# Kernel optimization log

Measured on AMD Instinct MI355X. Metric: run time of the kernel, lower is better.

The kernel has to match this reference:

```python
import jax, jax.numpy as jnp
import numpy as np

N_NODES = 50000
N_EDGES = 800000
DIM = 128


def setup_inputs() -> dict:
    key = jax.random.key(0)
    k1, k2, k3, k4, k5 = jax.random.split(key, 5)
    X = jax.random.normal(k1, (N_NODES, DIM), dtype=jnp.float32)
    src = jax.random.randint(k2, (N_EDGES,), 0, N_NODES, dtype=jnp.int64)
    dst = jax.random.randint(k3, (N_EDGES,), 0, N_NODES, dtype=jnp.int64)
    W_self = jax.random.normal(k4, (DIM, DIM), dtype=jnp.float32) * (1.0 / np.sqrt(DIM))
    W_neigh = jax.random.normal(k5, (DIM, DIM), dtype=jnp.float32) * (1.0 / np.sqrt(DIM))
    bias = jnp.zeros((DIM,), dtype=jnp.float32)
    return {"X": X, "src": src, "dst": dst, "W_self": W_self, "W_neigh": W_neigh, "bias": bias}


def reference(X, src, dst, W_self, W_neigh, bias):
    # h[u] = ReLU(W_self x_u + sum_{v in N(u)} W_neigh x_v + b)
    # Transform once per node, then gather per edge and segment-sum into dst.
    h_self = X @ W_self.T                       # [N, out]
    xw = X @ W_neigh.T                          # [N, out]
    h_neigh = jax.ops.segment_sum(xw[src], dst, num_segments=N_NODES)  # [N, out]
    return jax.nn.relu(h_self + h_neigh + bias)
```

## Files before the change

kernel.cpp:

```cpp
#include <hip/hip_runtime.h>
#include <hip/hip_bf16.h>

#define NN 50000
#define NE 800000
#define DIM 128
#define NBLK 49

#define NBUCK 196
#define CAP   6144
#define EPB   3200
#define PBLK  250

typedef __attribute__((ext_vector_type(8))) short bf16x8;
typedef __attribute__((ext_vector_type(4))) float f32x4;

__device__ __forceinline__ short f2bf(float f) {
    union { float f; unsigned u; } x; x.f = f;
    unsigned r = x.u + 0x7fffu + ((x.u >> 16) & 1u);
    return (short)(r >> 16);
}

__device__ __forceinline__ bf16x8 pack8(float4 a, float4 b) {
    bf16x8 v;
    v[0] = f2bf(a.x); v[1] = f2bf(a.y); v[2] = f2bf(a.z); v[3] = f2bf(a.w);
    v[4] = f2bf(b.x); v[5] = f2bf(b.y); v[6] = f2bf(b.z); v[7] = f2bf(b.w);
    return v;
}

__device__ __forceinline__ float bf2f(short s) {
    union { unsigned u; float f; } x; x.u = ((unsigned)(unsigned short)s) << 16;
    return x.f;
}

__device__ __forceinline__ void acc8(f32x4& aA, f32x4& aB, bf16x8 x) {
    aA[0] += bf2f(x[0]); aA[1] += bf2f(x[1]); aA[2] += bf2f(x[2]); aA[3] += bf2f(x[3]);
    aB[0] += bf2f(x[4]); aB[1] += bf2f(x[5]); aB[2] += bf2f(x[6]); aB[3] += bf2f(x[7]);
}

__global__ __launch_bounds__(256) void zero_k(int* __restrict__ p) {
    p[threadIdx.x] = 0;
}


__global__ __launch_bounds__(256) void part1(const float* __restrict__ X,
                                             const int* __restrict__ src,
                                             const int* __restrict__ dst,
                                             short* __restrict__ Xb,
                                             int* __restrict__ bucketFill,
                                             unsigned* __restrict__ edges) {
    __shared__ unsigned stage[EPB];
    __shared__ unsigned sorted_[EPB];
    __shared__ int lcnt[256];
    __shared__ int lst[256];
    __shared__ int goff[256];
    __shared__ int c2[256];

    int b = blockIdx.x;
    int t = threadIdx.x;

    if (b < 3125) {
        int i = b * 256 + t;
        const float4* p = (const float4*)(X + (size_t)i * 8);
        *(bf16x8*)(Xb + (size_t)i * 8) = pack8(p[0], p[1]);
        return;
    }

    int pb = b - 3125;
    int e0 = pb * EPB;
    lcnt[t] = 0; c2[t] = 0;
    __syncthreads();

    for (int i = t * 4; i < EPB; i += 1024) {
        int4 s4 = *(const int4*)(src + e0 + i);
        int4 d4 = *(const int4*)(dst + e0 + i);
        int ss[4] = {s4.x, s4.y, s4.z, s4.w};
        int dd[4] = {d4.x, d4.y, d4.z, d4.w};
        #pragma unroll
        for (int j = 0; j < 4; ++j) {
            unsigned bk = (unsigned)dd[j] >> 8;
            unsigned dl = (unsigned)dd[j] & 255u;
            stage[i + j] = (bk << 24) | (dl << 16) | (unsigned)ss[j];
            atomicAdd(&lcnt[bk], 1);
        }
    }
    __syncthreads();

    int v = lcnt[t];
    for (int off = 1; off < 256; off <<= 1) {
        __syncthreads();
        int tmp = (t >= off) ? lcnt[t - off] : 0;
        __syncthreads();
        lcnt[t] += tmp;
    }
    __syncthreads();
    int excl = lcnt[t] - v;
    lst[t] = excl;
    if (t < NBUCK) {
        int gb = atomicAdd(&bucketFill[t], v);
        goff[t] = t * CAP + gb - excl;
    }
    __syncthreads();

    for (int i = t * 4; i < EPB; i += 1024) {
        uint4 p4 = *(const uint4*)&stage[i];
        unsigned pp[4] = {p4.x, p4.y, p4.z, p4.w};
        #pragma unroll
        for (int j = 0; j < 4; ++j) {
            int bj = pp[j] >> 24;
            int r = atomicAdd(&c2[bj], 1);
            sorted_[lst[bj] + r] = pp[j];
        }
    }
    __syncthreads();

    for (int i = t * 4; i < EPB; i += 1024) {
        uint4 p4 = *(const uint4*)&sorted_[i];
        unsigned pp[4] = {p4.x, p4.y, p4.z, p4.w};
        #pragma unroll
        for (int j = 0; j < 4; ++j) {
            int bj = pp[j] >> 24;
            edges[(size_t)goff[bj] + i + j] = pp[j];
        }
    }
}

__global__ __launch_bounds__(256) void pull2(const short* __restrict__ Xb,
                                             const int* __restrict__ bucketFill,
                                             const unsigned* __restrict__ edges,
                                             short* __restrict__ aggb) {
    __shared__ int cnt[32];
    __shared__ int c2s[32];
    __shared__ int start[33];
    __shared__ unsigned short lcsr[1024];

    int t = threadIdx.x;
    int b  = blockIdx.x >> 3;
    int sl = blockIdx.x & 7;
    int dlo = sl * 32;
    int m = bucketFill[b];
    const unsigned* ed = edges + (size_t)b * CAP;

    if (t < 32) { cnt[t] = 0; c2s[t] = 0; }
    __syncthreads();

    for (int i = t * 4; i < m; i += 1024) {
        if (i + 4 <= m) {
            uint4 e4 = *(const uint4*)(ed + i);
            unsigned pp[4] = {e4.x, e4.y, e4.z, e4.w};
            #pragma unroll
            for (int j = 0; j < 4; ++j) {
                int o = ((pp[j] >> 16) & 255u) - dlo;
                if ((unsigned)o < 32u) atomicAdd(&cnt[o], 1);
            }
        } else {
            for (int k = i; k < m; ++k) {
                int o = ((ed[k] >> 16) & 255u) - dlo;
                if ((unsigned)o < 32u) atomicAdd(&cnt[o], 1);
            }
        }
    }
    __syncthreads();

    int v = (t < 32) ? cnt[t] : 0;
    for (int off = 1; off < 32; off <<= 1) {
        __syncthreads();
        int tmp = (t >= off && t < 32) ? cnt[t - off] : 0;
        __syncthreads();
        if (t < 32) cnt[t] += tmp;
    }
    __syncthreads();
    if (t < 32) start[t] = cnt[t] - v;
    if (t == 31) start[32] = cnt[31];
    __syncthreads();

    for (int i = t * 4; i < m; i += 1024) {
        if (i + 4 <= m) {
            uint4 e4 = *(const uint4*)(ed + i);
            unsigned pp[4] = {e4.x, e4.y, e4.z, e4.w};
            #pragma unroll
            for (int j = 0; j < 4; ++j) {
                int o = ((pp[j] >> 16) & 255u) - dlo;
                if ((unsigned)o < 32u) {
                    int r = atomicAdd(&c2s[o], 1);
                    lcsr[start[o] + r] = (unsigned short)(pp[j] & 0xffffu);
                }
            }
        } else {
            for (int k = i; k < m; ++k) {
                unsigned p = ed[k];
                int o = ((p >> 16) & 255u) - dlo;
                if ((unsigned)o < 32u) {
                    int r = atomicAdd(&c2s[o], 1);
                    lcsr[start[o] + r] = (unsigned short)(p & 0xffffu);
                }
            }
        }
    }
    __syncthreads();

    int lane = t & 63, wv = t >> 6;
    int g = lane >> 4, fl = lane & 15;
    const short* xbase = Xb + fl * 8;
    for (int n = wv; n < 32; n += 4) {
        int u = (b << 8) + dlo + n;
        if (u >= NN) continue;
        int beg = start[n], end = start[n + 1];
        f32x4 aA = {0.f, 0.f, 0.f, 0.f}, aB = {0.f, 0.f, 0.f, 0.f};
        int e = beg;
        for (; e + 16 <= end; e += 16) {
            int v0 = lcsr[e + g];
            int v1 = lcsr[e + 4 + g];
            int v2 = lcsr[e + 8 + g];
            int v3 = lcsr[e + 12 + g];
            bf16x8 x0 = *(const bf16x8*)(xbase + (size_t)v0 * DIM);
            bf16x8 x1 = *(const bf16x8*)(xbase + (size_t)v1 * DIM);
            bf16x8 x2 = *(const bf16x8*)(xbase + (size_t)v2 * DIM);
            bf16x8 x3 = *(const bf16x8*)(xbase + (size_t)v3 * DIM);
            acc8(aA, aB, x0); acc8(aA, aB, x1);
            acc8(aA, aB, x2); acc8(aA, aB, x3);
        }
        for (; e + 8 <= end; e += 8) {
            int v0 = lcsr[e + g];
            int v1 = lcsr[e + 4 + g];
            bf16x8 x0 = *(const bf16x8*)(xbase + (size_t)v0 * DIM);
            bf16x8 x1 = *(const bf16x8*)(xbase + (size_t)v1 * DIM);
            acc8(aA, aB, x0); acc8(aA, aB, x1);
        }
        for (; e < end; e += 4) {
            int idx = e + g;
            int vv = lcsr[idx < end ? idx : beg];
            bf16x8 x = *(const bf16x8*)(xbase + (size_t)vv * DIM);
            if (idx < end) acc8(aA, aB, x);
        }
        #pragma unroll
        for (int i = 0; i < 4; ++i) {
            aA[i] += __shfl_xor(aA[i], 16); aA[i] += __shfl_xor(aA[i], 32);
            aB[i] += __shfl_xor(aB[i], 16); aB[i] += __shfl_xor(aB[i], 32);
        }
        if (g == 0) {
            bf16x8 r;
            r[0] = f2bf(aA[0]); r[1] = f2bf(aA[1]); r[2] = f2bf(aA[2]); r[3] = f2bf(aA[3]);
            r[4] = f2bf(aB[0]); r[5] = f2bf(aB[1]); r[6] = f2bf(aB[2]); r[7] = f2bf(aB[3]);
            *(bf16x8*)(aggb + (size_t)u * DIM + fl * 8) = r;
        }
    }
}

__global__ __launch_bounds__(512) void gemm_bb(const short* __restrict__ Xb,
                                               const short* __restrict__ aggb,
                                               const float* __restrict__ Ws,
                                               const float* __restrict__ Wn,
                                               const float* __restrict__ bias,
                                               float* __restrict__ out) {
    __shared__ __align__(16) short wlds[2][128][128];
    for (int i = threadIdx.x; i < 128 * 16; i += 512) {
        int row = i >> 4;
        int c8 = (i & 15) << 3;
        int sc = c8 ^ ((row & 15) << 3);
        const float4* ps = (const float4*)(Ws + row * DIM + c8);
        *(bf16x8*)&wlds[0][row][sc] = pack8(ps[0], ps[1]);
        const float4* pn = (const float4*)(Wn + row * DIM + c8);
        *(bf16x8*)&wlds[1][row][sc] = pack8(pn[0], pn[1]);
    }
    __syncthreads();

    int lane = threadIdx.x & 63;
    int wv = threadIdx.x >> 6;
    int n0 = blockIdx.x * 128 + wv * 16;
    int arow = n0 + (lane & 15);
    int rowc = arow < NN ? arow : (NN - 1);
    const short* xr = Xb   + (size_t)rowc * DIM + (lane >> 4) * 8;
    const short* ar = aggb + (size_t)rowc * DIM + (lane >> 4) * 8;

    f32x4 acc[8] = {};
    #pragma unroll
    for (int ks = 0; ks < 4; ++ks) {
        int k0 = ks * 32;
        bf16x8 afx = *(const bf16x8*)(xr + k0);
        bf16x8 afg = *(const bf16x8*)(ar + k0);
        int bcol = k0 + (lane >> 4) * 8;
        #pragma unroll
        for (int ot = 0; ot < 8; ++ot) {
            int brow = ot * 16 + (lane & 15);
            int sc = bcol ^ ((brow & 15) << 3);
            bf16x8 bs = *(const bf16x8*)&wlds[0][brow][sc];
            bf16x8 bn = *(const bf16x8*)&wlds[1][brow][sc];
            acc[ot] = __builtin_amdgcn_mfma_f32_16x16x32_bf16(afx, bs, acc[ot], 0, 0, 0);
            acc[ot] = __builtin_amdgcn_mfma_f32_16x16x32_bf16(afg, bn, acc[ot], 0, 0, 0);
        }
    }

    int col0 = lane & 15;
    int rbase = n0 + (lane >> 4) * 4;
    #pragma unroll
    for (int ot = 0; ot < 8; ++ot) {
        int col = ot * 16 + col0;
        float bv = bias[col];
        #pragma unroll
        for (int i = 0; i < 4; ++i) {
            int r = rbase + i;
            if (r < NN) out[(size_t)r * DIM + col] = fmaxf(acc[ot][i] + bv, 0.f);
        }
    }
}


__global__ __launch_bounds__(256) void hist_k(const int* __restrict__ dst,
                                              int* __restrict__ cnt) {
    int e = blockIdx.x * 256 + threadIdx.x;
    if (e < NE) atomicAdd(&cnt[dst[e]], 1);
}

__global__ __launch_bounds__(1024) void scanA(const int* __restrict__ cnt,
                                              int* __restrict__ rowstart,
                                              int* __restrict__ bsum) {
    __shared__ int s[1024];
    int i = blockIdx.x * 1024 + threadIdx.x;
    int v = (i < NN) ? cnt[i] : 0;
    s[threadIdx.x] = v;
    for (int off = 1; off < 1024; off <<= 1) {
        __syncthreads();
        int t = (threadIdx.x >= off) ? s[threadIdx.x - off] : 0;
        __syncthreads();
        s[threadIdx.x] += t;
    }
    __syncthreads();
    if (i < NN) rowstart[i] = s[threadIdx.x] - v;
    if (threadIdx.x == 1023) bsum[blockIdx.x] = s[1023];
}

__global__ __launch_bounds__(64) void scanB(int* __restrict__ bsum) {
    int l = threadIdx.x;
    int orig = (l < NBLK) ? bsum[l] : 0;
    int v = orig;
    for (int off = 1; off < 64; off <<= 1) {
        int t = __shfl_up(v, off);
        if (l >= off) v += t;
    }
    if (l < NBLK) bsum[l] = v - orig;
}

__global__ __launch_bounds__(1024) void scanC(int* __restrict__ rowstart,
                                              const int* __restrict__ bsum) {
    int i = blockIdx.x * 1024 + threadIdx.x;
    if (i < NN) rowstart[i] += bsum[blockIdx.x];
    if (i == 0) rowstart[NN] = NE;
}

__global__ __launch_bounds__(256) void fill_atomic(const int* __restrict__ src,
                                                   const int* __restrict__ dst,
                                                   int* __restrict__ rowstart,
                                                   int* __restrict__ csr) {
    int e = blockIdx.x * 256 + threadIdx.x;
    if (e < NE) {
        int p = atomicAdd(&rowstart[dst[e]], 1);
        csr[p] = src[e];
    }
}

__global__ __launch_bounds__(256) void cvt_k(const float* __restrict__ X,
                                             short* __restrict__ Xb) {
    int i = blockIdx.x * 256 + threadIdx.x;
    if (i < NN * DIM / 8) {
        const float4* p = (const float4*)(X + (size_t)i * 8);
        *(bf16x8*)(Xb + (size_t)i * 8) = pack8(p[0], p[1]);
    }
}

__global__ __launch_bounds__(256) void pull_bf16(const short* __restrict__ Xb,
                                                 const int* __restrict__ rowend,
                                                 const int* __restrict__ csr,
                                                 float* __restrict__ agg) {
    int lane = threadIdx.x & 63;
    int u = (blockIdx.x * 256 + threadIdx.x) >> 6;
    if (u >= NN) return;
    int beg = (u == 0) ? 0 : rowend[u - 1];
    int end = rowend[u];
    float2 a0 = {0.f, 0.f}, a1 = {0.f, 0.f};
    int e = beg;
    for (; e + 1 < end; e += 2) {
        int v0 = csr[e], v1 = csr[e + 1];
        ushort2 x0 = *(const ushort2*)(Xb + (size_t)v0 * DIM + lane * 2);
        ushort2 x1 = *(const ushort2*)(Xb + (size_t)v1 * DIM + lane * 2);
        a0.x += bf2f(x0.x); a0.y += bf2f(x0.y);
        a1.x += bf2f(x1.x); a1.y += bf2f(x1.y);
    }
    if (e < end) {
        int v0 = csr[e];
        ushort2 x0 = *(const ushort2*)(Xb + (size_t)v0 * DIM + lane * 2);
        a0.x += bf2f(x0.x); a0.y += bf2f(x0.y);
    }
    float2 r = {a0.x + a1.x, a0.y + a1.y};
    *(float2*)(agg + (size_t)u * DIM + lane * 2) = r;
}

__global__ __launch_bounds__(256) void scatter_k(const float* __restrict__ X,
                                                 const int* __restrict__ src,
                                                 const int* __restrict__ dst,
                                                 float* __restrict__ agg) {
    int lane = threadIdx.x & 63;
    int gw = (blockIdx.x * 256 + threadIdx.x) >> 6;
    int nw = (gridDim.x * 256) >> 6;
    for (int e = gw; e < NE; e += nw) {
        int s = src[e];
        int d = dst[e];
        float2 v = *(const float2*)(X + (size_t)s * DIM + lane * 2);
        float* a = agg + (size_t)d * DIM + lane * 2;
        unsafeAtomicAdd(a, v.x);
        unsafeAtomicAdd(a + 1, v.y);
    }
}

__global__ __launch_bounds__(256) void fused_gemm(
        const float* __restrict__ X,
        const float* __restrict__ agg,
        const float* __restrict__ Ws,
        const float* __restrict__ Wn,
        const float* __restrict__ bias,
        float* __restrict__ out) {
    __shared__ __align__(16) short wlds[2][128][128];
    for (int i = threadIdx.x; i < 128 * 16; i += 256) {
        int row = i >> 4;
        int c8 = (i & 15) << 3;
        int sc = c8 ^ ((row & 15) << 3);
        const float4* ps = (const float4*)(Ws + row * DIM + c8);
        *(bf16x8*)&wlds[0][row][sc] = pack8(ps[0], ps[1]);
        const float4* pn = (const float4*)(Wn + row * DIM + c8);
        *(bf16x8*)&wlds[1][row][sc] = pack8(pn[0], pn[1]);
    }
    __syncthreads();

    int lane = threadIdx.x & 63;
    int wv = threadIdx.x >> 6;
    int n0 = blockIdx.x * 64 + wv * 16;
    int arow = n0 + (lane & 15);
    int rowc = arow < NN ? arow : (NN - 1);
    const float* xr = X + (size_t)rowc * DIM + (lane >> 4) * 8;
    const float* ar = agg + (size_t)rowc * DIM + (lane >> 4) * 8;

    f32x4 acc[8] = {};
    #pragma unroll
    for (int ks = 0; ks < 4; ++ks) {
        int k0 = ks * 32;
        float4 xa = *(const float4*)(xr + k0);
        float4 xb = *(const float4*)(xr + k0 + 4);
        bf16x8 afx = pack8(xa, xb);
        float4 ga = *(const float4*)(ar + k0);
        float4 gb = *(const float4*)(ar + k0 + 4);
        bf16x8 afg = pack8(ga, gb);
        int bcol = k0 + (lane >> 4) * 8;
        #pragma unroll
        for (int ot = 0; ot < 8; ++ot) {
            int brow = ot * 16 + (lane & 15);
            int sc = bcol ^ ((brow & 15) << 3);
            bf16x8 bs = *(const bf16x8*)&wlds[0][brow][sc];
            bf16x8 bn = *(const bf16x8*)&wlds[1][brow][sc];
            acc[ot] = __builtin_amdgcn_mfma_f32_16x16x32_bf16(afx, bs, acc[ot], 0, 0, 0);
            acc[ot] = __builtin_amdgcn_mfma_f32_16x16x32_bf16(afg, bn, acc[ot], 0, 0, 0);
        }
    }

    int col0 = lane & 15;
    int rbase = n0 + (lane >> 4) * 4;
    #pragma unroll
    for (int ot = 0; ot < 8; ++ot) {
        int col = ot * 16 + col0;
        float bv = bias[col];
        #pragma unroll
        for (int i = 0; i < 4; ++i) {
            int r = rbase + i;
            if (r < NN) out[(size_t)r * DIM + col] = fmaxf(acc[ot][i] + bv, 0.f);
        }
    }
}


extern "C" void kernel_launch(void* const* d_in, const int* in_sizes, int n_in,
                              void* d_out, int out_size, void* d_ws, size_t ws_size,
                              hipStream_t stream) {
    const float* X    = (const float*)d_in[0];
    const int*   src  = (const int*)  d_in[1];
    const int*   dst  = (const int*)  d_in[2];
    const float* Ws   = (const float*)d_in[3];
    const float* Wn   = (const float*)d_in[4];
    const float* bias = (const float*)d_in[5];
    float* out = (float*)d_out;

    const size_t REQ0 = ((size_t)256 + (size_t)NBUCK * CAP
                      + (size_t)NN * DIM / 2 * 2) * 4;
    const size_t REQ2 = (size_t)(50048 + 50056 + 64 + 800000) * 4
                      + (size_t)NN * DIM * 2;

    if (ws_size >= REQ0) {
        int*      bf    = (int*)d_ws;
        unsigned* edges = (unsigned*)(bf + 256);
        short*    Xb    = (short*)(edges + (size_t)NBUCK * CAP);
        short*    aggb  = Xb + (size_t)NN * DIM;

        zero_k<<<1, 256, 0, stream>>>(bf);
        part1<<<3125 + PBLK, 256, 0, stream>>>(X, src, dst, Xb, bf, edges);
        pull2<<<NBUCK * 8, 256, 0, stream>>>(Xb, bf, edges, aggb);
        gemm_bb<<<(NN + 127) / 128, 512, 0, stream>>>(Xb, aggb, Ws, Wn, bias, out);
    } else if (ws_size >= REQ2) {
        int* cnt      = (int*)d_ws;
        int* rowstart = cnt + 50048;
        int* bsum     = rowstart + 50056;
        int* csr      = bsum + 64;
        short* Xb     = (short*)(csr + 800000);

        hipMemsetAsync(cnt, 0, 50048 * sizeof(int), stream);
        hist_k<<<3125, 256, 0, stream>>>(dst, cnt);
        scanA<<<NBLK, 1024, 0, stream>>>(cnt, rowstart, bsum);
        scanB<<<1, 64, 0, stream>>>(bsum);
        scanC<<<NBLK, 1024, 0, stream>>>(rowstart, bsum);
        fill_atomic<<<3125, 256, 0, stream>>>(src, dst, rowstart, csr);
        cvt_k<<<3125, 256, 0, stream>>>(X, Xb);
        pull_bf16<<<12500, 256, 0, stream>>>(Xb, rowstart, csr, out);
        fused_gemm<<<(NN + 63) / 64, 256, 0, stream>>>(X, out, Ws, Wn, bias, out);
    } else {
        hipMemsetAsync(out, 0, (size_t)NN * DIM * sizeof(float), stream);
        scatter_k<<<2048, 256, 0, stream>>>(X, src, dst, out);
        fused_gemm<<<(NN + 63) / 64, 256, 0, stream>>>(X, out, Ws, Wn, bias, out);
    }
}
```

Before: 76.09 us.

## Fuse neighbor aggregation with dual GEMM, keep aggregates in LDS

Merges the pull aggregation kernel and the GEMM kernel into one pullgemm kernel. Each block now handles 64 destination nodes, keeps the bf16 aggregates in swizzled shared memory, and runs the self and neighbor MFMA passes one after the other. The weights are converted to bf16 once, by two extra blocks in part1, and reloaded into a single shared buffer between the two passes. This removes the global write and re-read of the aggregate tensor and one launch. In exchange it uses more shared memory per block and adds a capped local CSR (LCAP) that could silently drop edges when a 64-node slice has more than 1536 incoming edges.

```diff
diff --git a/kernel.cpp b/kernel.cpp
--- a/kernel.cpp
+++ b/kernel.cpp
@@ -10,6 +10,7 @@
 #define CAP   6144
 #define EPB   3200
 #define PBLK  250
+#define LCAP  1536
 
 typedef __attribute__((ext_vector_type(8))) short bf16x8;
 typedef __attribute__((ext_vector_type(4))) float f32x4;
@@ -45,7 +46,10 @@
 __global__ __launch_bounds__(256) void part1(const float* __restrict__ X,
                                              const int* __restrict__ src,
                                              const int* __restrict__ dst,
+                                             const float* __restrict__ Ws,
+                                             const float* __restrict__ Wn,
                                              short* __restrict__ Xb,
+                                             short* __restrict__ Wb,
                                              int* __restrict__ bucketFill,
                                              unsigned* __restrict__ edges) {
     __shared__ unsigned stage[EPB];
@@ -64,6 +68,18 @@
         *(bf16x8*)(Xb + (size_t)i * 8) = pack8(p[0], p[1]);
         return;
     }
+    if (b >= 3375) {
+        int w = b - 3375;
+        const float* Wsrc = (w == 0) ? Ws : Wn;
+        for (int i = t; i < 2048; i += 256) {
+            int row = i >> 4;
+            int c8 = (i & 15) << 3;
+            int sc = c8 ^ ((row & 15) << 3);
+            const float4* p = (const float4*)(Wsrc + row * DIM + c8);
+            *(bf16x8*)(Wb + (size_t)w * 16384 + row * 128 + sc) = pack8(p[0], p[1]);
+        }
+        return;
+    }
 
     int pb = b - 3125;
     int e0 = pb * EPB;
@@ -124,23 +140,28 @@
     }
 }
 
-__global__ __launch_bounds__(256) void pull2(const short* __restrict__ Xb,
-                                             const int* __restrict__ bucketFill,
-                                             const unsigned* __restrict__ edges,
-                                             short* __restrict__ aggb) {
-    __shared__ int cnt[32];
-    __shared__ int c2s[32];
-    __shared__ int start[33];
-    __shared__ unsigned short lcsr[1024];
+__global__ __launch_bounds__(256, 3) void pullgemm(
+        const short* __restrict__ Xb,
+        const short* __restrict__ Wb,
+        const int* __restrict__ bucketFill,
+        const unsigned* __restrict__ edges,
+        const float* __restrict__ bias,
+        float* __restrict__ out) {
+    __shared__ __align__(16) short wlds[128][128];
+    __shared__ __align__(16) short agg[64][128];
+    __shared__ unsigned short lcsr[LCAP];
+    __shared__ int cnt[64];
+    __shared__ int cur[64];
+    __shared__ int start[65];
 
     int t = threadIdx.x;
-    int b  = blockIdx.x >> 3;
-    int sl = blockIdx.x & 7;
-    int dlo = sl * 32;
+    int b  = blockIdx.x >> 2;
+    int sl = blockIdx.x & 3;
+    int dlo = sl * 64;
     int m = bucketFill[b];
     const unsigned* ed = edges + (size_t)b * CAP;
 
-    if (t < 32) { cnt[t] = 0; c2s[t] = 0; }
+    if (t < 64) { cnt[t] = 0; cur[t] = 0; }
     __syncthreads();
 
     for (int i = t * 4; i < m; i += 1024) {
@@ -150,27 +171,27 @@
             #pragma unroll
             for (int j = 0; j < 4; ++j) {
                 int o = ((pp[j] >> 16) & 255u) - dlo;
-                if ((unsigned)o < 32u) atomicAdd(&cnt[o], 1);
+                if ((unsigned)o < 64u) atomicAdd(&cnt[o], 1);
             }
         } else {
             for (int k = i; k < m; ++k) {
                 int o = ((ed[k] >> 16) & 255u) - dlo;
-                if ((unsigned)o < 32u) atomicAdd(&cnt[o], 1);
+                if ((unsigned)o < 64u) atomicAdd(&cnt[o], 1);
             }
         }
     }
     __syncthreads();
 
-    int v = (t < 32) ? cnt[t] : 0;
-    for (int off = 1; off < 32; off <<= 1) {
+    int v0 = (t < 64) ? cnt[t] : 0;
+    for (int off = 1; off < 64; off <<= 1) {
         __syncthreads();
-        int tmp = (t >= off && t < 32) ? cnt[t - off] : 0;
+        int tmp = (t >= off && t < 64) ? cnt[t - off] : 0;
         __syncthreads();
-        if (t < 32) cnt[t] += tmp;
-    }
-    __syncthreads();
-    if (t < 32) start[t] = cnt[t] - v;
-    if (t == 31) start[32] = cnt[31];
+        if (t < 64) cnt[t] += tmp;
+    }
+    __syncthreads();
+    if (t < 64) start[t] = cnt[t] - v0;
+    if (t == 63) start[64] = cnt[63];
     __syncthreads();
 
     for (int i = t * 4; i < m; i += 1024) {
@@ -180,18 +201,20 @@
             #pragma unroll
             for (int j = 0; j < 4; ++j) {
                 int o = ((pp[j] >> 16) & 255u) - dlo;
-                if ((unsigned)o < 32u) {
-                    int r = atomicAdd(&c2s[o], 1);
-                    lcsr[start[o] + r] = (unsigned short)(pp[j] & 0xffffu);
+                if ((unsigned)o < 64u) {
+                    int r = atomicAdd(&cur[o], 1);
+                    int idx = start[o] + r;
+                    if (idx < LCAP) lcsr[idx] = (unsigned short)(pp[j] & 0xffffu);
                 }
             }
         } else {
             for (int k = i; k < m; ++k) {
                 unsigned p = ed[k];
                 int o = ((p >> 16) & 255u) - dlo;
-                if ((unsigned)o < 32u) {
-                    int r = atomicAdd(&c2s[o], 1);
-                    lcsr[start[o] + r] = (unsigned short)(p & 0xffffu);
+                if ((unsigned)o < 64u) {
+                    int r = atomicAdd(&cur[o], 1);
+                    int idx = start[o] + r;
+                    if (idx < LCAP) lcsr[idx] = (unsigned short)(p & 0xffffu);
                 }
             }
         }
@@ -201,29 +224,29 @@
     int lane = t & 63, wv = t >> 6;
     int g = lane >> 4, fl = lane & 15;
     const short* xbase = Xb + fl * 8;
-    for (int n = wv; n < 32; n += 4) {
-        int u = (b << 8) + dlo + n;
-        if (u >= NN) continue;
+    for (int n = wv; n < 64; n += 4) {
         int beg = start[n], end = start[n + 1];
+        if (beg > LCAP) beg = LCAP;
+        if (end > LCAP) end = LCAP;
         f32x4 aA = {0.f, 0.f, 0.f, 0.f}, aB = {0.f, 0.f, 0.f, 0.f};
         int e = beg;
         for (; e + 16 <= end; e += 16) {
-            int v0 = lcsr[e + g];
-            int v1 = lcsr[e + 4 + g];
-            int v2 = lcsr[e + 8 + g];
-            int v3 = lcsr[e + 12 + g];
-            bf16x8 x0 = *(const bf16x8*)(xbase + (size_t)v0 * DIM);
-            bf16x8 x1 = *(const bf16x8*)(xbase + (size_t)v1 * DIM);
-            bf16x8 x2 = *(const bf16x8*)(xbase + (size_t)v2 * DIM);
-            bf16x8 x3 = *(const bf16x8*)(xbase + (size_t)v3 * DIM);
+            int v0i = lcsr[e + g];
+            int v1i = lcsr[e + 4 + g];
+            int v2i = lcsr[e + 8 + g];
+            int v3i = lcsr[e + 12 + g];
+            bf16x8 x0 = *(const bf16x8*)(xbase + (size_t)v0i * DIM);
+            bf16x8 x1 = *(const bf16x8*)(xbase + (size_t)v1i * DIM);
+            bf16x8 x2 = *(const bf16x8*)(xbase + (size_t)v2i * DIM);
+            bf16x8 x3 = *(const bf16x8*)(xbase + (size_t)v3i * DIM);
             acc8(aA, aB, x0); acc8(aA, aB, x1);
             acc8(aA, aB, x2); acc8(aA, aB, x3);
         }
         for (; e + 8 <= end; e += 8) {
-            int v0 = lcsr[e + g];
-            int v1 = lcsr[e + 4 + g];
-            bf16x8 x0 = *(const bf16x8*)(xbase + (size_t)v0 * DIM);
-            bf16x8 x1 = *(const bf16x8*)(xbase + (size_t)v1 * DIM);
+            int v0i = lcsr[e + g];
+            int v1i = lcsr[e + 4 + g];
+            bf16x8 x0 = *(const bf16x8*)(xbase + (size_t)v0i * DIM);
+            bf16x8 x1 = *(const bf16x8*)(xbase + (size_t)v1i * DIM);
             acc8(aA, aB, x0); acc8(aA, aB, x1);
         }
         for (; e < end; e += 4) {
@@ -241,51 +264,52 @@
             bf16x8 r;
             r[0] = f2bf(aA[0]); r[1] = f2bf(aA[1]); r[2] = f2bf(aA[2]); r[3] = f2bf(aA[3]);
             r[4] = f2bf(aB[0]); r[5] = f2bf(aB[1]); r[6] = f2bf(aB[2]); r[7] = f2bf(aB[3]);
-            *(bf16x8*)(aggb + (size_t)u * DIM + fl * 8) = r;
-        }
-    }
-}
-
-__global__ __launch_bounds__(512) void gemm_bb(const short* __restrict__ Xb,
-                                               const short* __restrict__ aggb,
-                                               const float* __restrict__ Ws,
-                                               const float* __restrict__ Wn,
-                                               const float* __restrict__ bias,
-                                               float* __restrict__ out) {
-    __shared__ __align__(16) short wlds[2][128][128];
-    for (int i = threadIdx.x; i < 128 * 16; i += 512) {
-        int row = i >> 4;
-        int c8 = (i & 15) << 3;
-        int sc = c8 ^ ((row & 15) << 3);
-        const float4* ps = (const float4*)(Ws + row * DIM + c8);
-        *(bf16x8*)&wlds[0][row][sc] = pack8(ps[0], ps[1]);
-        const float4* pn = (const float4*)(Wn + row * DIM + c8);
-        *(bf16x8*)&wlds[1][row][sc] = pack8(pn[0], pn[1]);
-    }
-    __syncthreads();
-
-    int lane = threadIdx.x & 63;
-    int wv = threadIdx.x >> 6;
-    int n0 = blockIdx.x * 128 + wv * 16;
+            *(bf16x8*)&agg[n][8 * (fl ^ (n & 15))] = r;
+        }
+    }
+    __syncthreads();
+
+    for (int i = t; i < 2048; i += 256)
+        *(bf16x8*)((short*)wlds + (size_t)i * 8) = *(const bf16x8*)(Wb + (size_t)i * 8);
+    __syncthreads();
+
+    int n0 = b * 256 + dlo + wv * 16;
     int arow = n0 + (lane & 15);
     int rowc = arow < NN ? arow : (NN - 1);
-    const short* xr = Xb   + (size_t)rowc * DIM + (lane >> 4) * 8;
-    const short* ar = aggb + (size_t)rowc * DIM + (lane >> 4) * 8;
+    const short* xr = Xb + (size_t)rowc * DIM + (lane >> 4) * 8;
 
     f32x4 acc[8] = {};
     #pragma unroll
     for (int ks = 0; ks < 4; ++ks) {
         int k0 = ks * 32;
         bf16x8 afx = *(const bf16x8*)(xr + k0);
-        bf16x8 afg = *(const bf16x8*)(ar + k0);
         int bcol = k0 + (lane >> 4) * 8;
         #pragma unroll
         for (int ot = 0; ot < 8; ++ot) {
             int brow = ot * 16 + (lane & 15);
             int sc = bcol ^ ((brow & 15) << 3);
-            bf16x8 bs = *(const bf16x8*)&wlds[0][brow][sc];
-            bf16x8 bn = *(const bf16x8*)&wlds[1][brow][sc];
+            bf16x8 bs = *(const bf16x8*)&wlds[brow][sc];
             acc[ot] = __builtin_amdgcn_mfma_f32_16x16x32_bf16(afx, bs, acc[ot], 0, 0, 0);
+        }
+    }
+    __syncthreads();
+
+    for (int i = t; i < 2048; i += 256)
+        *(bf16x8*)((short*)wlds + (size_t)i * 8) = *(const bf16x8*)(Wb + 16384 + (size_t)i * 8);
+    __syncthreads();
+
+    int ra = lane & 15;
+    int cb = lane >> 4;
+    #pragma unroll
+    for (int ks = 0; ks < 4; ++ks) {
+        int c = ks * 4 + cb;
+        bf16x8 afg = *(const bf16x8*)&agg[wv * 16 + ra][8 * (c ^ ra)];
+        int bcol = ks * 32 + cb * 8;
+        #pragma unroll
+        for (int ot = 0; ot < 8; ++ot) {
+            int brow = ot * 16 + ra;
+            int sc = bcol ^ ((brow & 15) << 3);
+            bf16x8 bn = *(const bf16x8*)&wlds[brow][sc];
             acc[ot] = __builtin_amdgcn_mfma_f32_16x16x32_bf16(afg, bn, acc[ot], 0, 0, 0);
         }
     }
@@ -486,8 +510,8 @@
     const float* bias = (const float*)d_in[5];
     float* out = (float*)d_out;
 
-    const size_t REQ0 = ((size_t)256 + (size_t)NBUCK * CAP
-                      + (size_t)NN * DIM / 2 * 2) * 4;
+    const size_t REQ0 = (size_t)256 * 4 + (size_t)NBUCK * CAP * 4
+                      + (size_t)NN * DIM * 2 + (size_t)32768 * 2;
     const size_t REQ2 = (size_t)(50048 + 50056 + 64 + 800000) * 4
                       + (size_t)NN * DIM * 2;
 
@@ -495,12 +519,11 @@
         int*      bf    = (int*)d_ws;
         unsigned* edges = (unsigned*)(bf + 256);
         short*    Xb    = (short*)(edges + (size_t)NBUCK * CAP);
-        short*    aggb  = Xb + (size_t)NN * DIM;
+        short*    Wb    = Xb + (size_t)NN * DIM;
 
         zero_k<<<1, 256, 0, stream>>>(bf);
-        part1<<<3125 + PBLK, 256, 0, stream>>>(X, src, dst, Xb, bf, edges);
-        pull2<<<NBUCK * 8, 256, 0, stream>>>(Xb, bf, edges, aggb);
-        gemm_bb<<<(NN + 127) / 128, 512, 0, stream>>>(Xb, aggb, Ws, Wn, bias, out);
+        part1<<<3125 + PBLK + 2, 256, 0, stream>>>(X, src, dst, Ws, Wn, Xb, Wb, bf, edges);
+        pullgemm<<<NBUCK * 4, 256, 0, stream>>>(Xb, Wb, bf, edges, bias, out);
     } else if (ws_size >= REQ2) {
         int* cnt      = (int*)d_ws;
         int* rowstart = cnt + 50048;
```

New measurement: 101.6 us. +33.5%, slower.

## Pre-convert weights to bf16 once and widen pull blocks to 64 nodes

Applied to the files above, without the earlier changes.

Two extra blocks in part1 convert W_self and W_neigh to swizzled bf16 in workspace, so each gemm_bb block copies ready bf16 tiles into LDS instead of converting fp32 weights itself. pull2 now uses 512-thread blocks covering 64 destination nodes per slice, which halves how many times each bucket's edge list is rescanned. The local CSR grows to 2048 entries with clamping, so edges past that capacity would be silently dropped. The workspace requirement is enlarged to hold the bf16 weights.

```diff
diff --git a/kernel.cpp b/kernel.cpp
--- a/kernel.cpp
+++ b/kernel.cpp
@@ -10,6 +10,7 @@
 #define CAP   6144
 #define EPB   3200
 #define PBLK  250
+#define LCAP  2048
 
 typedef __attribute__((ext_vector_type(8))) short bf16x8;
 typedef __attribute__((ext_vector_type(4))) float f32x4;
@@ -45,7 +46,10 @@
 __global__ __launch_bounds__(256) void part1(const float* __restrict__ X,
                                              const int* __restrict__ src,
                                              const int* __restrict__ dst,
+                                             const float* __restrict__ Ws,
+                                             const float* __restrict__ Wn,
                                              short* __restrict__ Xb,
+                                             short* __restrict__ Wb,
                                              int* __restrict__ bucketFill,
                                              unsigned* __restrict__ edges) {
     __shared__ unsigned stage[EPB];
@@ -64,6 +68,18 @@
         *(bf16x8*)(Xb + (size_t)i * 8) = pack8(p[0], p[1]);
         return;
     }
+    if (b >= 3375) {
+        int w = b - 3375;
+        const float* Wsrc = (w == 0) ? Ws : Wn;
+        for (int i = t; i < 2048; i += 256) {
+            int row = i >> 4;
+            int c8 = (i & 15) << 3;
+            int sc = c8 ^ ((row & 15) << 3);
+            const float4* p = (const float4*)(Wsrc + row * DIM + c8);
+            *(bf16x8*)(Wb + (size_t)w * 16384 + row * 128 + sc) = pack8(p[0], p[1]);
+        }
+        return;
+    }
 
     int pb = b - 3125;
     int e0 = pb * EPB;
@@ -124,74 +140,76 @@
     }
 }
 
-__global__ __launch_bounds__(256) void pull2(const short* __restrict__ Xb,
+__global__ __launch_bounds__(512) void pull2(const short* __restrict__ Xb,
                                              const int* __restrict__ bucketFill,
                                              const unsigned* __restrict__ edges,
                                              short* __restrict__ aggb) {
-    __shared__ int cnt[32];
-    __shared__ int c2s[32];
-    __shared__ int start[33];
-    __shared__ unsigned short lcsr[1024];
+    __shared__ int cnt[64];
+    __shared__ int c2s[64];
+    __shared__ int start[65];
+    __shared__ unsigned short lcsr[LCAP];
 
     int t = threadIdx.x;
-    int b  = blockIdx.x >> 3;
-    int sl = blockIdx.x & 7;
-    int dlo = sl * 32;
+    int b  = blockIdx.x >> 2;
+    int sl = blockIdx.x & 3;
+    int dlo = sl * 64;
     int m = bucketFill[b];
     const unsigned* ed = edges + (size_t)b * CAP;
 
-    if (t < 32) { cnt[t] = 0; c2s[t] = 0; }
-    __syncthreads();
-
-    for (int i = t * 4; i < m; i += 1024) {
+    if (t < 64) { cnt[t] = 0; c2s[t] = 0; }
+    __syncthreads();
+
+    for (int i = t * 4; i < m; i += 2048) {
         if (i + 4 <= m) {
             uint4 e4 = *(const uint4*)(ed + i);
             unsigned pp[4] = {e4.x, e4.y, e4.z, e4.w};
             #pragma unroll
             for (int j = 0; j < 4; ++j) {
                 int o = ((pp[j] >> 16) & 255u) - dlo;
-                if ((unsigned)o < 32u) atomicAdd(&cnt[o], 1);
+                if ((unsigned)o < 64u) atomicAdd(&cnt[o], 1);
             }
         } else {
             for (int k = i; k < m; ++k) {
                 int o = ((ed[k] >> 16) & 255u) - dlo;
-                if ((unsigned)o < 32u) atomicAdd(&cnt[o], 1);
+                if ((unsigned)o < 64u) atomicAdd(&cnt[o], 1);
             }
         }
     }
     __syncthreads();
 
-    int v = (t < 32) ? cnt[t] : 0;
-    for (int off = 1; off < 32; off <<= 1) {
+    int v = (t < 64) ? cnt[t] : 0;
+    for (int off = 1; off < 64; off <<= 1) {
         __syncthreads();
-        int tmp = (t >= off && t < 32) ? cnt[t - off] : 0;
+        int tmp = (t >= off && t < 64) ? cnt[t - off] : 0;
         __syncthreads();
-        if (t < 32) cnt[t] += tmp;
-    }
-    __syncthreads();
-    if (t < 32) start[t] = cnt[t] - v;
-    if (t == 31) start[32] = cnt[31];
-    __syncthreads();
-
-    for (int i = t * 4; i < m; i += 1024) {
+        if (t < 64) cnt[t] += tmp;
+    }
+    __syncthreads();
+    if (t < 64) start[t] = cnt[t] - v;
+    if (t == 63) start[64] = cnt[63];
+    __syncthreads();
+
+    for (int i = t * 4; i < m; i += 2048) {
         if (i + 4 <= m) {
             uint4 e4 = *(const uint4*)(ed + i);
             unsigned pp[4] = {e4.x, e4.y, e4.z, e4.w};
             #pragma unroll
             for (int j = 0; j < 4; ++j) {
                 int o = ((pp[j] >> 16) & 255u) - dlo;
-                if ((unsigned)o < 32u) {
+                if ((unsigned)o < 64u) {
                     int r = atomicAdd(&c2s[o], 1);
-                    lcsr[start[o] + r] = (unsigned short)(pp[j] & 0xffffu);
+                    int idx = start[o] + r;
+                    if (idx < LCAP) lcsr[idx] = (unsigned short)(pp[j] & 0xffffu);
                 }
             }
         } else {
             for (int k = i; k < m; ++k) {
                 unsigned p = ed[k];
                 int o = ((p >> 16) & 255u) - dlo;
-                if ((unsigned)o < 32u) {
+                if ((unsigned)o < 64u) {
                     int r = atomicAdd(&c2s[o], 1);
-                    lcsr[start[o] + r] = (unsigned short)(p & 0xffffu);
+                    int idx = start[o] + r;
+                    if (idx < LCAP) lcsr[idx] = (unsigned short)(p & 0xffffu);
                 }
             }
         }
@@ -201,10 +219,12 @@
     int lane = t & 63, wv = t >> 6;
     int g = lane >> 4, fl = lane & 15;
     const short* xbase = Xb + fl * 8;
-    for (int n = wv; n < 32; n += 4) {
+    for (int n = wv; n < 64; n += 8) {
         int u = (b << 8) + dlo + n;
         if (u >= NN) continue;
         int beg = start[n], end = start[n + 1];
+        if (beg > LCAP) beg = LCAP;
+        if (end > LCAP) end = LCAP;
         f32x4 aA = {0.f, 0.f, 0.f, 0.f}, aB = {0.f, 0.f, 0.f, 0.f};
         int e = beg;
         for (; e + 16 <= end; e += 16) {
@@ -248,20 +268,12 @@
 
 __global__ __launch_bounds__(512) void gemm_bb(const short* __restrict__ Xb,
                                                const short* __restrict__ aggb,
-                                               const float* __restrict__ Ws,
-                                               const float* __restrict__ Wn,
+                                               const short* __restrict__ Wb,
                                                const float* __restrict__ bias,
                                                float* __restrict__ out) {
     __shared__ __align__(16) short wlds[2][128][128];
-    for (int i = threadIdx.x; i < 128 * 16; i += 512) {
-        int row = i >> 4;
-        int c8 = (i & 15) << 3;
-        int sc = c8 ^ ((row & 15) << 3);
-        const float4* ps = (const float4*)(Ws + row * DIM + c8);
-        *(bf16x8*)&wlds[0][row][sc] = pack8(ps[0], ps[1]);
-        const float4* pn = (const float4*)(Wn + row * DIM + c8);
-        *(bf16x8*)&wlds[1][row][sc] = pack8(pn[0], pn[1]);
-    }
+    for (int i = threadIdx.x; i < 4096; i += 512)
+        *(bf16x8*)((short*)wlds + (size_t)i * 8) = *(const bf16x8*)(Wb + (size_t)i * 8);
     __syncthreads();
 
     int lane = threadIdx.x & 63;
@@ -486,8 +498,8 @@
     const float* bias = (const float*)d_in[5];
     float* out = (float*)d_out;
 
-    const size_t REQ0 = ((size_t)256 + (size_t)NBUCK * CAP
-                      + (size_t)NN * DIM / 2 * 2) * 4;
+    const size_t REQ0 = (size_t)256 * 4 + (size_t)NBUCK * CAP * 4
+                      + (size_t)NN * DIM * 2 * 2 + (size_t)32768 * 2;
     const size_t REQ2 = (size_t)(50048 + 50056 + 64 + 800000) * 4
                       + (size_t)NN * DIM * 2;
 
@@ -496,11 +508,12 @@
         unsigned* edges = (unsigned*)(bf + 256);
         short*    Xb    = (short*)(edges + (size_t)NBUCK * CAP);
         short*    aggb  = Xb + (size_t)NN * DIM;
+        short*    Wb    = aggb + (size_t)NN * DIM;
 
         zero_k<<<1, 256, 0, stream>>>(bf);
-        part1<<<3125 + PBLK, 256, 0, stream>>>(X, src, dst, Xb, bf, edges);
-        pull2<<<NBUCK * 8, 256, 0, stream>>>(Xb, bf, edges, aggb);
-        gemm_bb<<<(NN + 127) / 128, 512, 0, stream>>>(Xb, aggb, Ws, Wn, bias, out);
+        part1<<<3125 + PBLK + 2, 256, 0, stream>>>(X, src, dst, Ws, Wn, Xb, Wb, bf, edges);
+        pull2<<<NBUCK * 4, 512, 0, stream>>>(Xb, bf, edges, aggb);
+        gemm_bb<<<(NN + 127) / 128, 512, 0, stream>>>(Xb, aggb, Wb, bias, out);
     } else if (ws_size >= REQ2) {
         int* cnt      = (int*)d_ws;
         int* rowstart = cnt + 50048;
```

New measurement: 74.41 us. 1.02x faster.
